# Kernel tuning notes

Measured on AMD Instinct MI355X. Metric: run time of the kernel, lower is better.

The kernel has to match this reference:

```python
import jax, jax.numpy as jnp
import numpy as np
import math

B, L, D, H, FF = 32, 512, 512, 8, 2048
DH = D // H
EPS = 1e-5

def pe_table(L, D):
    pos = jnp.arange(L, dtype=jnp.float32)[:, None]
    div = jnp.exp(jnp.arange(0, D, 2, dtype=jnp.float32) * (-(math.log(10000.0) / D)))
    pe = jnp.zeros((L, D), dtype=jnp.float32)
    pe = pe.at[:, 0::2].set(jnp.sin(pos * div))
    pe = pe.at[:, 1::2].set(jnp.cos(pos * div))
    return pe

def setup_inputs() -> dict:
    key = jax.random.key(0)
    ks = jax.random.split(key, 16)
    s = 0.02
    inp = {
        "x": jax.random.normal(ks[0], (B, L, D), jnp.float32),
        "mask": jnp.ones((B, L), jnp.int32),
        "speaker_emb": jax.random.normal(ks[1], (B, L, D), jnp.float32),
        "Wg": jax.random.normal(ks[2], (D, D), jnp.float32) * s,
        "Wq": jax.random.normal(ks[3], (D, D), jnp.float32) * s,
        "bq": jnp.zeros((D,), jnp.float32),
        "Wk": jax.random.normal(ks[4], (D, D), jnp.float32) * s,
        "bk": jnp.zeros((D,), jnp.float32),
        "Wv": jax.random.normal(ks[5], (D, D), jnp.float32) * s,
        "bv": jnp.zeros((D,), jnp.float32),
        "Wo": jax.random.normal(ks[6], (D, D), jnp.float32) * s,
        "bo": jnp.zeros((D,), jnp.float32),
        "ln_g": jnp.ones((D,), jnp.float32),
        "ln_b": jnp.zeros((D,), jnp.float32),
        "W1": jax.random.normal(ks[7], (FF, D), jnp.float32) * s,
        "b1": jnp.zeros((FF,), jnp.float32),
        "W2": jax.random.normal(ks[8], (D, FF), jnp.float32) * s,
        "b2": jnp.zeros((D,), jnp.float32),
    }
    return inp

def layer_norm(x, g, b):
    mu = jnp.mean(x, axis=-1, keepdims=True)
    var = jnp.var(x, axis=-1, keepdims=True)
    return (x - mu) * jax.lax.rsqrt(var + EPS) * g + b

def reference(x, mask, speaker_emb, Wg, Wq, bq, Wk, bk, Wv, bv, Wo, bo, ln_g, ln_b, W1, b1, W2, b2):
    # DynamicGating: sigmoid(x W^T) * x
    x = jax.nn.sigmoid(x @ Wg.T) * x
    # speaker embedding + sinusoidal positional encoding (dropout is eval/no-op)
    x = x + speaker_emb + pe_table(L, D)[None, :, :]
    # Multi-head self-attention (eager, full score matrix)
    q = (x @ Wq.T + bq).reshape(B, L, H, DH).transpose(0, 2, 1, 3) / math.sqrt(DH)
    k = (x @ Wk.T + bk).reshape(B, L, H, DH).transpose(0, 2, 1, 3)
    v = (x @ Wv.T + bv).reshape(B, L, H, DH).transpose(0, 2, 1, 3)
    scores = jnp.einsum("bhqd,bhkd->bhqk", q, k)  # (B,H,L,L)
    key_mask = (mask == 0)[:, None, None, :]  # mask keys where mask==0
    scores = jnp.where(key_mask, jnp.float32(-1e10), scores)
    attn = jax.nn.softmax(scores, axis=-1)
    ctx = jnp.einsum("bhqk,bhkd->bhqd", attn, v)
    ctx = ctx.transpose(0, 2, 1, 3).reshape(B, L, D)
    attn_out = ctx @ Wo.T + bo
    h = attn_out + x  # residual (dropout no-op)
    # FeedForwardNet: note GELU applied after BOTH linears (faithful to source)
    mid = jax.nn.gelu(layer_norm(h, ln_g, ln_b) @ W1.T + b1, approximate=True)
    out = jax.nn.gelu(mid @ W2.T + b2, approximate=True)
    return out + h
```

## Files before the change

kernel.cpp:

```cpp
#include <hip/hip_runtime.h>
#include <math.h>

#define Bn 32
#define Ln 512
#define Dn 512
#define Hn 8
#define DHn 64
#define FFn 2048
#define Mn (Bn*Ln)
#define QKVS 1536

typedef __attribute__((ext_vector_type(4))) float f32x4;
typedef __attribute__((ext_vector_type(8))) short short8;

__device__ __forceinline__ float bf2f(ushort u){ return __uint_as_float(((unsigned)u) << 16); }
__device__ __forceinline__ ushort f2bf(float f){
  unsigned u = __float_as_uint(f);
  u += 0x7FFFu + ((u >> 16) & 1u);
  return (ushort)(u >> 16);
}
__device__ __forceinline__ float gelu_fast(float x){
  float y2 = 1.5957691216057308f * (x + 0.044715f*x*x*x);
  return x / (1.0f + __expf(-y2));
}

__device__ __forceinline__ void gload_lds16(const ushort* g, ushort* l){
  __builtin_amdgcn_global_load_lds(
      (__attribute__((address_space(1))) void*)(void*)g,
      (__attribute__((address_space(3))) void*)(void*)l, 16, 0, 0);
}

__device__ __forceinline__ void cvt4(const float* __restrict__ in, ushort* __restrict__ out, int u){
  float4 v = *(const float4*)(in + u*4);
  ushort4 o;
  o.x = f2bf(v.x); o.y = f2bf(v.y); o.z = f2bf(v.z); o.w = f2bf(v.w);
  *(ushort4*)(out + u*4) = o;
}

__global__ __launch_bounds__(256) void prep_kernel(
    const float* __restrict__ Wg, const float* __restrict__ Wq, const float* __restrict__ Wk,
    const float* __restrict__ Wv, const float* __restrict__ Wo, const float* __restrict__ W1,
    const float* __restrict__ W2,
    const float* __restrict__ bq, const float* __restrict__ bk, const float* __restrict__ bv,
    ushort* __restrict__ wgb, ushort* __restrict__ wqkvb, ushort* __restrict__ wob,
    ushort* __restrict__ w1b, ushort* __restrict__ w2b,
    float* __restrict__ pe, float* __restrict__ bqkv)
{
  int u = blockIdx.x*256 + threadIdx.x;
  const int WU = 65536, FU = 262144;
  if (u < WU){ cvt4(Wg, wgb, u); return; }            u -= WU;
  if (u < WU){ cvt4(Wq, wqkvb, u); return; }          u -= WU;
  if (u < WU){ cvt4(Wk, wqkvb + 262144, u); return; } u -= WU;
  if (u < WU){ cvt4(Wv, wqkvb + 524288, u); return; } u -= WU;
  if (u < WU){ cvt4(Wo, wob, u); return; }            u -= WU;
  if (u < FU){ cvt4(W1, w1b, u); return; }            u -= FU;
  if (u < FU){ cvt4(W2, w2b, u); return; }            u -= FU;
  if (u < WU){
    int e = u*4; int l = e >> 9; int d0 = e & 511;
    #pragma unroll
    for (int p=0;p<2;p++){
      int i = (d0 >> 1) + p;
      float dv = expf((float)(2*i) * (-9.210340371976184f/512.0f));
      float ang = (float)l * dv;
      pe[e + 2*p]     = sinf(ang);
      pe[e + 2*p + 1] = cosf(ang);
    }
    return;
  }
  u -= WU;
  if (u < 384){
    int e = u*4;
    #pragma unroll
    for (int j=0;j<4;j++){
      int i = e + j;
      bqkv[i] = (i < 512) ? bq[i] : (i < 1024) ? bk[i-512] : bv[i-1024];
    }
  }
}

__global__ void cvt_kernel(const float* __restrict__ in, ushort* __restrict__ out, int n){
  int i = (blockIdx.x*256 + threadIdx.x)*4;
  if (i >= n) return;
  cvt4(in, out, i >> 2);
}

template<int MODE>
__global__ __launch_bounds__(256) void gemm_kernel(
    const ushort* __restrict__ A, const ushort* __restrict__ W,
    const float* __restrict__ bias,
    const float* __restrict__ res,
    const float* __restrict__ spk, const float* __restrict__ pe,
    float* __restrict__ outf, ushort* __restrict__ outb, ushort* __restrict__ outb2,
    int K, int N, int gx)
{
  __shared__ ushort lA[2][128][64];
  __shared__ ushort lW[2][128][64];
  int t = threadIdx.x;
  int wave = t >> 6, lane = t & 63;
  int wr = wave >> 1, wc = wave & 1;
  int g = lane >> 4, r16 = lane & 15;

  int nwg = gx * (Mn/128);
  int wg = blockIdx.x;
  int tile = (wg & 7)*(nwg >> 3) + (wg >> 3);
  int trow = tile / gx;
  int tcol = tile - trow*gx;
  int rowBase = trow * 128;
  int colBase = tcol * 128;

  int srow8 = lane >> 3;
  int sucol = ((lane & 7) ^ srow8) * 8;
  const ushort* gA = A + (size_t)(rowBase + wave*8 + srow8)*K + sucol;
  const ushort* gW = W + (size_t)(colBase + wave*8 + srow8)*K + sucol;

  f32x4 acc[4][4];
  #pragma unroll
  for (int m=0;m<4;m++)
    #pragma unroll
    for (int n=0;n<4;n++) acc[m][n] = (f32x4)0.0f;

  {
    ushort* la = &lA[0][0][0] + wave*512;
    ushort* lw = &lW[0][0][0] + wave*512;
    #pragma unroll
    for (int c=0;c<4;c++){
      gload_lds16(gA + (size_t)c*32*K, la + c*2048);
      gload_lds16(gW + (size_t)c*32*K, lw + c*2048);
    }
  }
  __syncthreads();

  int cb = 0;
  for (int k0 = 0; k0 < K; k0 += 64){
    if (k0 + 64 < K){
      ushort* la = &lA[cb^1][0][0] + wave*512;
      ushort* lw = &lW[cb^1][0][0] + wave*512;
      #pragma unroll
      for (int c=0;c<4;c++){
        gload_lds16(gA + (size_t)c*32*K + k0 + 64, la + c*2048);
        gload_lds16(gW + (size_t)c*32*K + k0 + 64, lw + c*2048);
      }
    }
    #pragma unroll
    for (int ks=0; ks<2; ks++){
      short8 af[4], bfr[4];
      #pragma unroll
      for (int m=0;m<4;m++){
        int row = wr*64 + m*16 + r16;
        af[m] = *(const short8*)&lA[cb][row][(((ks<<2)+g) ^ (r16 & 7))*8];
      }
      #pragma unroll
      for (int n=0;n<4;n++){
        int row = wc*64 + n*16 + r16;
        bfr[n] = *(const short8*)&lW[cb][row][(((ks<<2)+g) ^ (r16 & 7))*8];
      }
      #pragma unroll
      for (int m=0;m<4;m++)
        #pragma unroll
        for (int n=0;n<4;n++)
          acc[m][n] = __builtin_amdgcn_mfma_f32_16x16x32_bf16(af[m], bfr[n], acc[m][n], 0, 0, 0);
    }
    __syncthreads();
    cb ^= 1;
  }

  #pragma unroll
  for (int m=0;m<4;m++){
    #pragma unroll
    for (int n=0;n<4;n++){
      int gc = colBase + wc*64 + n*16 + r16;
      if constexpr (MODE == 1){
        if (gc < 1024){
          float sc = (gc < 512) ? 0.125f : 1.0f;
          #pragma unroll
          for (int j=0;j<4;j++){
            int gr = rowBase + wr*64 + m*16 + g*4 + j;
            outb[(size_t)gr*N + gc] = f2bf((acc[m][n][j] + bias[gc]) * sc);
          }
        } else {
          int dhg = gc - 1024;
          int gr0 = rowBase + wr*64 + m*16 + g*4;
          int bb = gr0 >> 9, l0 = gr0 & 511;
          ushort4 o4;
          o4.x = f2bf(acc[m][n][0] + bias[gc]);
          o4.y = f2bf(acc[m][n][1] + bias[gc]);
          o4.z = f2bf(acc[m][n][2] + bias[gc]);
          o4.w = f2bf(acc[m][n][3] + bias[gc]);
          *(ushort4*)(outb2 + ((size_t)(bb*Hn + (dhg>>6))*DHn + (dhg & 63))*Ln + l0) = o4;
        }
      } else {
        #pragma unroll
        for (int j=0;j<4;j++){
          int gr = rowBase + wr*64 + m*16 + g*4 + j;
          size_t o = (size_t)gr * N + gc;
          float c = acc[m][n][j];
          if constexpr (MODE == 0){
            float s = 1.0f/(1.0f + __expf(-c));
            float rv = s * res[o] + spk[o] + pe[(gr & (Ln-1))*Dn + gc];
            outf[o] = rv; outb[o] = f2bf(rv);
          } else if constexpr (MODE == 2){
            outf[o] = c + bias[gc] + res[o];
          } else if constexpr (MODE == 3){
            outb[o] = f2bf(gelu_fast(c + bias[gc]));
          } else {
            outf[o] = gelu_fast(c + bias[gc]) + res[o];
          }
        }
      }
    }
  }
}

__global__ __launch_bounds__(256) void attn_mfma_kernel(
    const ushort* __restrict__ qb, const ushort* __restrict__ kb, const ushort* __restrict__ vtb,
    const int* __restrict__ mask, ushort* __restrict__ ctxb)
{
  __shared__ ushort lK[2][64][72];
  __shared__ ushort lP[4][32][72];

  int t = threadIdx.x;
  int w = t >> 6, lane = t & 63;
  int g = lane >> 4, r16 = lane & 15;
  int b = blockIdx.z, h = blockIdx.y;
  int qbase = blockIdx.x*128 + w*32;

  int key0 = t >> 3, key1 = key0 + 32;
  int c8s = (t & 7) * 8;
  const ushort* kbase = kb + (size_t)(b*Ln)*QKVS + h*DHn + c8s;
  const ushort* vt = vtb + (size_t)((b*Hn + h)*DHn) * Ln;

  short8 af_q[2][2];
  #pragma unroll
  for (int m=0;m<2;m++)
    #pragma unroll
    for (int ks=0;ks<2;ks++)
      af_q[m][ks] = *(const short8*)(qb + (size_t)(b*Ln + qbase + m*16 + r16)*QKVS + h*DHn + ks*32 + g*8);

  f32x4 acc_ctx[2][4];
  #pragma unroll
  for (int m=0;m<2;m++)
    #pragma unroll
    for (int n=0;n<4;n++) acc_ctx[m][n] = (f32x4)0.0f;
  float mrun[2][4], lrun[2][4];
  #pragma unroll
  for (int m=0;m<2;m++)
    #pragma unroll
    for (int j=0;j<4;j++){ mrun[m][j] = -INFINITY; lrun[m][j] = 0.0f; }

  {
    short8 ka = *(const short8*)(kbase + (size_t)key0*QKVS);
    short8 kc = *(const short8*)(kbase + (size_t)key1*QKVS);
    *(short8*)&lK[0][key0][c8s] = ka;
    *(short8*)&lK[0][key1][c8s] = kc;
  }
  __syncthreads();
  int cb = 0;

  for (int kb0 = 0; kb0 < Ln; kb0 += 64){
    short8 kna, knb;
    bool more = (kb0 + 64 < Ln);
    if (more){
      kna = *(const short8*)(kbase + (size_t)(kb0 + 64 + key0)*QKVS);
      knb = *(const short8*)(kbase + (size_t)(kb0 + 64 + key1)*QKVS);
    }

    f32x4 acc_s[2][4];
    #pragma unroll
    for (int m=0;m<2;m++)
      #pragma unroll
      for (int n=0;n<4;n++) acc_s[m][n] = (f32x4)0.0f;
    __builtin_amdgcn_s_setprio(1);
    #pragma unroll
    for (int ks=0;ks<2;ks++){
      short8 bf_k[4];
      #pragma unroll
      for (int n=0;n<4;n++)
        bf_k[n] = *(const short8*)&lK[cb][n*16 + r16][ks*32 + g*8];
      #pragma unroll
      for (int m=0;m<2;m++)
        #pragma unroll
        for (int n=0;n<4;n++)
          acc_s[m][n] = __builtin_amdgcn_mfma_f32_16x16x32_bf16(af_q[m][ks], bf_k[n], acc_s[m][n], 0, 0, 0);
    }
    __builtin_amdgcn_s_setprio(0);

    #pragma unroll
    for (int n=0;n<4;n++){
      if (mask[b*Ln + kb0 + n*16 + r16] == 0){
        #pragma unroll
        for (int m=0;m<2;m++)
          #pragma unroll
          for (int j=0;j<4;j++) acc_s[m][n][j] = -1e10f;
      }
    }

    #pragma unroll
    for (int m=0;m<2;m++){
      #pragma unroll
      for (int j=0;j<4;j++){
        float tmax = fmaxf(fmaxf(acc_s[m][0][j], acc_s[m][1][j]),
                           fmaxf(acc_s[m][2][j], acc_s[m][3][j]));
        #pragma unroll
        for (int off=1; off<16; off<<=1) tmax = fmaxf(tmax, __shfl_xor(tmax, off));
        float newm = fmaxf(mrun[m][j], tmax);
        float alpha = __expf(mrun[m][j] - newm);
        float p0 = __expf(acc_s[m][0][j] - newm);
        float p1 = __expf(acc_s[m][1][j] - newm);
        float p2 = __expf(acc_s[m][2][j] - newm);
        float p3 = __expf(acc_s[m][3][j] - newm);
        float tsum = (p0+p1)+(p2+p3);
        #pragma unroll
        for (int off=1; off<16; off<<=1) tsum += __shfl_xor(tsum, off);
        lrun[m][j] = lrun[m][j]*alpha + tsum;
        mrun[m][j] = newm;
        #pragma unroll
        for (int n2=0;n2<4;n2++) acc_ctx[m][n2][j] *= alpha;
        int prow = m*16 + g*4 + j;
        lP[w][prow][0*16 + r16] = f2bf(p0);
        lP[w][prow][1*16 + r16] = f2bf(p1);
        lP[w][prow][2*16 + r16] = f2bf(p2);
        lP[w][prow][3*16 + r16] = f2bf(p3);
      }
    }

    __builtin_amdgcn_s_setprio(1);
    #pragma unroll
    for (int ks2=0;ks2<2;ks2++){
      short8 af_p[2], bf_v[4];
      #pragma unroll
      for (int m=0;m<2;m++)
        af_p[m] = *(const short8*)&lP[w][m*16 + r16][ks2*32 + g*8];
      #pragma unroll
      for (int n=0;n<4;n++)
        bf_v[n] = *(const short8*)(vt + (size_t)(n*16 + r16)*Ln + kb0 + ks2*32 + g*8);
      #pragma unroll
      for (int m=0;m<2;m++)
        #pragma unroll
        for (int n=0;n<4;n++)
          acc_ctx[m][n] = __builtin_amdgcn_mfma_f32_16x16x32_bf16(af_p[m], bf_v[n], acc_ctx[m][n], 0, 0, 0);
    }
    __builtin_amdgcn_s_setprio(0);

    if (more){
      *(short8*)&lK[cb^1][key0][c8s] = kna;
      *(short8*)&lK[cb^1][key1][c8s] = knb;
    }
    __syncthreads();
    cb ^= 1;
  }

  #pragma unroll
  for (int m=0;m<2;m++){
    #pragma unroll
    for (int j=0;j<4;j++){
      float inv = 1.0f / lrun[m][j];
      int gr = qbase + m*16 + g*4 + j;
      #pragma unroll
      for (int n=0;n<4;n++){
        ctxb[(size_t)(b*Ln + gr)*Dn + h*DHn + n*16 + r16] = f2bf(acc_ctx[m][n][j] * inv);
      }
    }
  }
}

__global__ __launch_bounds__(256) void ln_kernel(
    const float* __restrict__ hbuf, const float* __restrict__ gamma, const float* __restrict__ beta,
    ushort* __restrict__ out)
{
  int row = blockIdx.x*4 + (threadIdx.x >> 6);
  int lane = threadIdx.x & 63;
  const float* p = hbuf + (size_t)row*Dn + lane*8;
  float4 a = *(const float4*)p;
  float4 c = *(const float4*)(p + 4);
  float v[8] = {a.x,a.y,a.z,a.w,c.x,c.y,c.z,c.w};
  float s = 0.f, ss = 0.f;
  #pragma unroll
  for (int j=0;j<8;j++){ s += v[j]; ss += v[j]*v[j]; }
  #pragma unroll
  for (int off=32; off>0; off>>=1){ s += __shfl_xor(s, off); ss += __shfl_xor(ss, off); }
  float mu = s * (1.0f/Dn);
  float var = ss * (1.0f/Dn) - mu*mu;
  float rstd = rsqrtf(var + 1e-5f);
  ushort o8[8];
  #pragma unroll
  for (int j=0;j<8;j++) o8[j] = f2bf((v[j]-mu)*rstd*gamma[lane*8+j] + beta[lane*8+j]);
  ushort* op = out + (size_t)row*Dn + lane*8;
  *(ushort4*)op       = make_ushort4(o8[0],o8[1],o8[2],o8[3]);
  *(ushort4*)(op + 4) = make_ushort4(o8[4],o8[5],o8[6],o8[7]);
}

extern "C" void kernel_launch(void* const* d_in, const int* in_sizes, int n_in,
                              void* d_out, int out_size, void* d_ws, size_t ws_size,
                              hipStream_t stream) {
  (void)in_sizes; (void)n_in; (void)out_size; (void)ws_size;
  const float* x    = (const float*)d_in[0];
  const int*   mask = (const int*)d_in[1];
  const float* spk  = (const float*)d_in[2];
  const float* Wg   = (const float*)d_in[3];
  const float* Wq   = (const float*)d_in[4];  const float* bq = (const float*)d_in[5];
  const float* Wk   = (const float*)d_in[6];  const float* bk = (const float*)d_in[7];
  const float* Wv   = (const float*)d_in[8];  const float* bv = (const float*)d_in[9];
  const float* Wo   = (const float*)d_in[10]; const float* bo = (const float*)d_in[11];
  const float* lng  = (const float*)d_in[12]; const float* lnbeta = (const float*)d_in[13];
  const float* W1   = (const float*)d_in[14]; const float* b1 = (const float*)d_in[15];
  const float* W2   = (const float*)d_in[16]; const float* b2 = (const float*)d_in[17];
  float* out = (float*)d_out;

  char* w = (char*)d_ws;
  size_t o = 0;
  ushort* xbf   = (ushort*)(w + o); o += (size_t)Mn*Dn*2;
  ushort* xinb  = (ushort*)(w + o); o += (size_t)Mn*Dn*2;
  ushort* qkvb  = (ushort*)(w + o); o += (size_t)Mn*QKVS*2;
  ushort* vtb   = (ushort*)(w + o); o += (size_t)Mn*Dn*2;
  ushort* ctxb  = (ushort*)(w + o); o += (size_t)Mn*Dn*2;
  float*  xinf  = (float*)(w + o);  o += (size_t)Mn*Dn*4;
  float*  hbuf  = (float*)(w + o);  o += (size_t)Mn*Dn*4;
  ushort* lnbuf = (ushort*)(w + o); o += (size_t)Mn*Dn*2;
  ushort* wgb   = (ushort*)(w + o); o += (size_t)Dn*Dn*2;
  ushort* wqkvb = (ushort*)(w + o); o += (size_t)QKVS*Dn*2;
  ushort* wob   = (ushort*)(w + o); o += (size_t)Dn*Dn*2;
  ushort* w1b   = (ushort*)(w + o); o += (size_t)FFn*Dn*2;
  ushort* w2b   = (ushort*)(w + o); o += (size_t)Dn*FFn*2;
  float*  pebuf = (float*)(w + o);  o += (size_t)Ln*Dn*4;
  float*  bqkv  = (float*)(w + o);  o += (size_t)QKVS*4;
  ushort* midb  = xbf;

  hipLaunchKernelGGL(prep_kernel, dim3(3586), dim3(256), 0, stream,
                     Wg, Wq, Wk, Wv, Wo, W1, W2, bq, bk, bv,
                     wgb, wqkvb, wob, w1b, w2b, pebuf, bqkv);
  hipLaunchKernelGGL(cvt_kernel, dim3((Mn*Dn/4)/256), dim3(256), 0, stream, x, xbf, Mn*Dn);

  hipLaunchKernelGGL((gemm_kernel<0>), dim3((Dn/128)*(Mn/128)), dim3(256), 0, stream,
                     xbf, wgb, (const float*)nullptr, x, spk, pebuf, xinf, xinb, (ushort*)nullptr,
                     Dn, Dn, Dn/128);
  hipLaunchKernelGGL((gemm_kernel<1>), dim3((QKVS/128)*(Mn/128)), dim3(256), 0, stream,
                     xinb, wqkvb, bqkv, (const float*)nullptr, (const float*)nullptr, (const float*)nullptr,
                     (float*)nullptr, qkvb, vtb, Dn, QKVS, QKVS/128);
  hipLaunchKernelGGL(attn_mfma_kernel, dim3(Ln/128, Hn, Bn), dim3(256), 0, stream,
                     qkvb, qkvb + 512, vtb, mask, ctxb);
  hipLaunchKernelGGL((gemm_kernel<2>), dim3((Dn/128)*(Mn/128)), dim3(256), 0, stream,
                     ctxb, wob, bo, xinf, (const float*)nullptr, (const float*)nullptr,
                     hbuf, (ushort*)nullptr, (ushort*)nullptr, Dn, Dn, Dn/128);
  hipLaunchKernelGGL(ln_kernel, dim3(Mn/4), dim3(256), 0, stream, hbuf, lng, lnbeta, lnbuf);
  hipLaunchKernelGGL((gemm_kernel<3>), dim3((FFn/128)*(Mn/128)), dim3(256), 0, stream,
                     lnbuf, w1b, b1, (const float*)nullptr, (const float*)nullptr, (const float*)nullptr,
                     (float*)nullptr, midb, (ushort*)nullptr, Dn, FFn, FFn/128);
  hipLaunchKernelGGL((gemm_kernel<4>), dim3((Dn/128)*(Mn/128)), dim3(256), 0, stream,
                     midb, w2b, b2, hbuf, (const float*)nullptr, (const float*)nullptr,
                     out, (ushort*)nullptr, (ushort*)nullptr, FFn, Dn, Dn/128);
}
```

Baseline: 319.0 us.

## Stage GEMM bf16 epilogue through LDS and double-buffer V tiles in attention

For the QK projection part and the FFN1 GEMM, the output tile is first written into shared memory with an XOR swizzle, then stored to global memory as full 16-byte row-contiguous writes instead of scattered 2-byte stores. In the attention kernel, V^T tiles are prefetched into a double-buffered LDS array alongside K rather than each wave reading them straight from global memory. The aim is better write coalescing and fewer redundant global reads of V. The cost is an extra __syncthreads in the epilogue and more LDS per attention block, which may lower occupancy.

```diff
diff --git a/kernel.cpp b/kernel.cpp
--- a/kernel.cpp
+++ b/kernel.cpp
@@ -164,20 +164,44 @@
     cb ^= 1;
   }
 
-  #pragma unroll
-  for (int m=0;m<4;m++){
-    #pragma unroll
-    for (int n=0;n<4;n++){
-      int gc = colBase + wc*64 + n*16 + r16;
-      if constexpr (MODE == 1){
-        if (gc < 1024){
-          float sc = (gc < 512) ? 0.125f : 1.0f;
+  if constexpr (MODE == 1 || MODE == 3){
+    bool vpart = false;
+    if constexpr (MODE == 1) vpart = (colBase >= 1024);
+    if (!vpart){
+      ushort* ct = &lA[0][0][0];
+      #pragma unroll
+      for (int m=0;m<4;m++){
+        #pragma unroll
+        for (int n=0;n<4;n++){
+          int col = wc*64 + n*16 + r16;
+          int gc = colBase + col;
+          float sc = 1.0f;
+          if constexpr (MODE == 1) sc = (gc < 512) ? 0.125f : 1.0f;
           #pragma unroll
           for (int j=0;j<4;j++){
-            int gr = rowBase + wr*64 + m*16 + g*4 + j;
-            outb[(size_t)gr*N + gc] = f2bf((acc[m][n][j] + bias[gc]) * sc);
+            int row = wr*64 + m*16 + g*4 + j;
+            float c = acc[m][n][j] + bias[gc];
+            ushort val;
+            if constexpr (MODE == 3) val = f2bf(gelu_fast(c));
+            else                     val = f2bf(c * sc);
+            ct[row*128 + (col ^ ((row & 7) << 3))] = val;
           }
-        } else {
+        }
+      }
+      __syncthreads();
+      int r = t >> 1, ch = (t & 1)*64;
+      ushort* dst = outb + (size_t)(rowBase + r)*N + colBase + ch;
+      #pragma unroll
+      for (int q=0;q<8;q++){
+        int col = (ch + q*8) ^ ((r & 7) << 3);
+        *(short8*)(dst + q*8) = *(const short8*)&ct[r*128 + col];
+      }
+    } else {
+      #pragma unroll
+      for (int m=0;m<4;m++){
+        #pragma unroll
+        for (int n=0;n<4;n++){
+          int gc = colBase + wc*64 + n*16 + r16;
           int dhg = gc - 1024;
           int gr0 = rowBase + wr*64 + m*16 + g*4;
           int bb = gr0 >> 9, l0 = gr0 & 511;
@@ -188,7 +212,14 @@
           o4.w = f2bf(acc[m][n][3] + bias[gc]);
           *(ushort4*)(outb2 + ((size_t)(bb*Hn + (dhg>>6))*DHn + (dhg & 63))*Ln + l0) = o4;
         }
-      } else {
+      }
+    }
+  } else {
+    #pragma unroll
+    for (int m=0;m<4;m++){
+      #pragma unroll
+      for (int n=0;n<4;n++){
+        int gc = colBase + wc*64 + n*16 + r16;
         #pragma unroll
         for (int j=0;j<4;j++){
           int gr = rowBase + wr*64 + m*16 + g*4 + j;
@@ -200,8 +231,6 @@
             outf[o] = rv; outb[o] = f2bf(rv);
           } else if constexpr (MODE == 2){
             outf[o] = c + bias[gc] + res[o];
-          } else if constexpr (MODE == 3){
-            outb[o] = f2bf(gelu_fast(c + bias[gc]));
           } else {
             outf[o] = gelu_fast(c + bias[gc]) + res[o];
           }
@@ -216,6 +245,7 @@
     const int* __restrict__ mask, ushort* __restrict__ ctxb)
 {
   __shared__ ushort lK[2][64][72];
+  __shared__ ushort lVt[2][64][72];
   __shared__ ushort lP[4][32][72];
 
   int t = threadIdx.x;
@@ -224,7 +254,7 @@
   int b = blockIdx.z, h = blockIdx.y;
   int qbase = blockIdx.x*128 + w*32;
 
-  int key0 = t >> 3, key1 = key0 + 32;
+  int key0 = t >> 3;
   int c8s = (t & 7) * 8;
   const ushort* kbase = kb + (size_t)(b*Ln)*QKVS + h*DHn + c8s;
   const ushort* vt = vtb + (size_t)((b*Hn + h)*DHn) * Ln;
@@ -249,19 +279,25 @@
 
   {
     short8 ka = *(const short8*)(kbase + (size_t)key0*QKVS);
-    short8 kc = *(const short8*)(kbase + (size_t)key1*QKVS);
+    short8 kc = *(const short8*)(kbase + (size_t)(key0+32)*QKVS);
+    short8 va = *(const short8*)(vt + (size_t)key0*Ln + c8s);
+    short8 vc = *(const short8*)(vt + (size_t)(key0+32)*Ln + c8s);
     *(short8*)&lK[0][key0][c8s] = ka;
-    *(short8*)&lK[0][key1][c8s] = kc;
+    *(short8*)&lK[0][key0+32][c8s] = kc;
+    *(short8*)&lVt[0][key0][c8s] = va;
+    *(short8*)&lVt[0][key0+32][c8s] = vc;
   }
   __syncthreads();
   int cb = 0;
 
   for (int kb0 = 0; kb0 < Ln; kb0 += 64){
-    short8 kna, knb;
+    short8 kna, knb, vna, vnb;
     bool more = (kb0 + 64 < Ln);
     if (more){
       kna = *(const short8*)(kbase + (size_t)(kb0 + 64 + key0)*QKVS);
-      knb = *(const short8*)(kbase + (size_t)(kb0 + 64 + key1)*QKVS);
+      knb = *(const short8*)(kbase + (size_t)(kb0 + 64 + key0 + 32)*QKVS);
+      vna = *(const short8*)(vt + (size_t)key0*Ln + kb0 + 64 + c8s);
+      vnb = *(const short8*)(vt + (size_t)(key0+32)*Ln + kb0 + 64 + c8s);
     }
 
     f32x4 acc_s[2][4];
@@ -332,7 +368,7 @@
         af_p[m] = *(const short8*)&lP[w][m*16 + r16][ks2*32 + g*8];
       #pragma unroll
       for (int n=0;n<4;n++)
-        bf_v[n] = *(const short8*)(vt + (size_t)(n*16 + r16)*Ln + kb0 + ks2*32 + g*8);
+        bf_v[n] = *(const short8*)&lVt[cb][n*16 + r16][ks2*32 + g*8];
       #pragma unroll
       for (int m=0;m<2;m++)
         #pragma unroll
@@ -343,7 +379,9 @@
 
     if (more){
       *(short8*)&lK[cb^1][key0][c8s] = kna;
-      *(short8*)&lK[cb^1][key1][c8s] = knb;
+      *(short8*)&lK[cb^1][key0+32][c8s] = knb;
+      *(short8*)&lVt[cb^1][key0][c8s] = vna;
+      *(short8*)&lVt[cb^1][key0+32][c8s] = vnb;
     }
     __syncthreads();
     cb ^= 1;
```

Result: slower. 328.2 us (+2.9%).
